# Kernel optimization log

Measured on AMD Instinct MI355X. Metric: run time of the kernel, lower is better.

The kernel has to match this reference:

```python
import jax, jax.numpy as jnp
import numpy as np

B, N, C = 64, 196, 768
H = 12
HD = C // H            # 64
TOPK = int(0.25 * HD)  # 16
HIDDEN = int(C * 4.0)  # 3072
SCALE = HD ** -0.5
EPS = 1e-5


def layernorm(x, g, b):
    mu = jnp.mean(x, axis=-1, keepdims=True)
    var = jnp.var(x, axis=-1, keepdims=True)
    return (x - mu) * jax.lax.rsqrt(var + EPS) * g + b


def setup_inputs() -> dict:
    key = jax.random.key(0)
    ks = jax.random.split(key, 8)
    s = 0.02
    return {
        "x": jax.random.normal(ks[0], (B, N, C), jnp.float32),
        "norm1_g": jnp.ones((C,), jnp.float32),
        "norm1_b": jnp.zeros((C,), jnp.float32),
        "qk_w": jax.random.normal(ks[1], (2 * C, C), jnp.float32) * s,   # torch Linear [out,in], no bias
        "attn_proj_w": jax.random.normal(ks[2], (C, H * TOPK), jnp.float32) * s,
        "attn_proj_b": jnp.zeros((C,), jnp.float32),
        "norm2_g": jnp.ones((C,), jnp.float32),
        "norm2_b": jnp.zeros((C,), jnp.float32),
        "fc1_w": jax.random.normal(ks[3], (HIDDEN, C), jnp.float32) * s,
        "fc1_b": jnp.zeros((HIDDEN,), jnp.float32),
        "fc2_w": jax.random.normal(ks[4], (C, HIDDEN), jnp.float32) * s,
        "fc2_b": jnp.zeros((C,), jnp.float32),
    }


def reference(x, norm1_g, norm1_b, qk_w, attn_proj_w, attn_proj_b,
              norm2_g, norm2_b, fc1_w, fc1_b, fc2_w, fc2_b):
    # --- HomoAttention branch ---
    h = layernorm(x, norm1_g, norm1_b)                       # [B,N,C]
    qk = h @ qk_w.T                                          # [B,N,2C]
    qk = qk.reshape(B, N, 2, H, HD).transpose(2, 0, 3, 1, 4) # [2,B,H,N,HD]
    q, k = qk[0] * SCALE, qk[1]
    attn = jnp.einsum('bhnd,bhmd->bhnm', q, k)               # [B,H,N,N]
    top_vals, _ = jax.lax.top_k(attn, TOPK)                  # [B,H,N,TOPK]
    a = jax.nn.softmax(top_vals, axis=-1)
    a = a.transpose(0, 2, 1, 3).reshape(B, N, H * TOPK)      # [B,N,H*TOPK]
    x = x + a @ attn_proj_w.T + attn_proj_b

    # --- MLP branch ---
    h2 = layernorm(x, norm2_g, norm2_b)
    h2 = jax.nn.gelu(h2 @ fc1_w.T + fc1_b, approximate=False)
    x = x + h2 @ fc2_w.T + fc2_b
    return x
```

## Files before the change

### kernel.cpp

```cpp
#include <hip/hip_runtime.h>


#define BATCH 64
#define SEQ   196
#define CH    768
#define NHEAD 12
#define HDIM  64
#define TOPK  16
#define HID   3072
#define MROWS 12544
#define MHALF 6272
#define SCALE_F 0.125f
#define NEGBIG -3e38f

typedef __bf16 bf16x8 __attribute__((ext_vector_type(8)));
typedef float  f32x4  __attribute__((ext_vector_type(4)));

__device__ __forceinline__ unsigned short f2b(float f) {
    union { float f; unsigned int i; } c; c.f = f;
    unsigned int u = c.i;
    return (unsigned short)((u + 0x7fffu + ((u >> 16) & 1u)) >> 16);
}

__device__ __forceinline__ void async16(const unsigned short* g, unsigned short* l) {
    __builtin_amdgcn_global_load_lds(
        (const __attribute__((address_space(1))) unsigned int*)(g),
        (__attribute__((address_space(3))) unsigned int*)(l), 16, 0, 0);
}

__global__ __launch_bounds__(256) void f2b4_k(const float* __restrict__ s0, unsigned short* __restrict__ d0, int n0,
                                              const float* __restrict__ s1, unsigned short* __restrict__ d1, int n1,
                                              const float* __restrict__ s2, unsigned short* __restrict__ d2, int n2,
                                              const float* __restrict__ s3, unsigned short* __restrict__ d3, int n3)
{
    int idx = (blockIdx.x * 256 + threadIdx.x) * 4;
    const float* s; unsigned short* d; int n;
    if (idx < n0) { s = s0; d = d0; n = n0; }
    else {
        idx -= n0;
        if (idx < n1) { s = s1; d = d1; n = n1; }
        else {
            idx -= n1;
            if (idx < n2) { s = s2; d = d2; n = n2; }
            else { idx -= n2; s = s3; d = d3; n = n3; }
        }
    }
    if (idx < n) {
        float4 v = *(const float4*)(s + idx);
        ushort4 o;
        o.x = f2b(v.x); o.y = f2b(v.y); o.z = f2b(v.z); o.w = f2b(v.w);
        *(ushort4*)(d + idx) = o;
    }
}

__global__ __launch_bounds__(256) void ln_k(const float* __restrict__ x,
                                            const float* __restrict__ gw,
                                            const float* __restrict__ bw,
                                            unsigned short* __restrict__ out)
{
    const int row = blockIdx.x;
    const int tid = threadIdx.x;
    const float* xr = x + (size_t)row * CH;
    float v0 = xr[tid], v1 = xr[tid + 256], v2 = xr[tid + 512];
    float s  = v0 + v1 + v2;
    float sq = v0*v0 + v1*v1 + v2*v2;
#pragma unroll
    for (int off = 32; off > 0; off >>= 1) {
        s  += __shfl_down(s, off, 64);
        sq += __shfl_down(sq, off, 64);
    }
    __shared__ __align__(16) float red[8];
    if ((tid & 63) == 0) { red[(tid >> 6) * 2] = s; red[(tid >> 6) * 2 + 1] = sq; }
    __syncthreads();
    s  = red[0] + red[2] + red[4] + red[6];
    sq = red[1] + red[3] + red[5] + red[7];
    float mu  = s * (1.0f / CH);
    float var = sq * (1.0f / CH) - mu * mu;
    float rs  = rsqrtf(var + 1e-5f);
    unsigned short* orow = out + (size_t)row * CH;
    orow[tid]       = f2b((v0 - mu) * rs * gw[tid]       + bw[tid]);
    orow[tid + 256] = f2b((v1 - mu) * rs * gw[tid + 256] + bw[tid + 256]);
    orow[tid + 512] = f2b((v2 - mu) * rs * gw[tid + 512] + bw[tid + 512]);
}

template<bool BIAS, bool RES, bool GELU, bool OUTF>
__global__ __launch_bounds__(256, 3)
void gemm_bt64(const unsigned short* __restrict__ A,
               const unsigned short* __restrict__ Bw,
               const float* __restrict__ bias,
               const float* __restrict__ resid,
               void* __restrict__ Cout,
               int M, int N, int K)
{
    __shared__ __align__(16) unsigned short As[2][2][64 * 32];
    __shared__ __align__(16) unsigned short Bs[2][2][128 * 32];
    const int tid  = threadIdx.x;
    const int w    = tid >> 6;
    const int lane = tid & 63;
    const int tileN = blockIdx.x * 128;
    const int tileM = blockIdx.y * 64;
    const int wn = w * 32;
    const int q   = lane >> 4;
    const int l16 = lane & 15;

    f32x4 acc[4][2];
#pragma unroll
    for (int i = 0; i < 4; ++i)
#pragma unroll
        for (int j = 0; j < 2; ++j) acc[i][j] = (f32x4){0.f, 0.f, 0.f, 0.f};

    const int r0 = tid >> 2, c0 = (tid & 3) * 8;

    const int kIters = K >> 6;

    auto stage = [&](int kt, int buf) {
#pragma unroll
        for (int h = 0; h < 2; ++h) {
            const size_t koff = (size_t)kt * 64 + h * 32;
            async16(A + (size_t)(tileM + r0) * K + koff + c0,
                    &As[buf][h][(size_t)(w * 64) * 8]);
            async16(Bw + (size_t)(tileN + r0) * K + koff + c0,
                    &Bs[buf][h][(size_t)(w * 64) * 8]);
            async16(Bw + (size_t)(tileN + r0 + 64) * K + koff + c0,
                    &Bs[buf][h][(size_t)(256 + w * 64) * 8]);
        }
    };

    stage(0, 0);
    int cur = 0;
    for (int kt = 0; kt < kIters; ++kt) {
        __syncthreads();
        if (kt + 1 < kIters) stage(kt + 1, cur ^ 1);
#pragma unroll
        for (int h = 0; h < 2; ++h) {
            bf16x8 af[4], bfr[2];
#pragma unroll
            for (int i = 0; i < 4; ++i)
                af[i] = *(const bf16x8*)&As[cur][h][(i * 16 + l16) * 32 + q * 8];
#pragma unroll
            for (int j = 0; j < 2; ++j)
                bfr[j] = *(const bf16x8*)&Bs[cur][h][(wn + j * 16 + l16) * 32 + q * 8];
#pragma unroll
            for (int i = 0; i < 4; ++i)
#pragma unroll
                for (int j = 0; j < 2; ++j)
                    acc[i][j] = __builtin_amdgcn_mfma_f32_16x16x32_bf16(af[i], bfr[j], acc[i][j], 0, 0, 0);
        }
        cur ^= 1;
    }

#pragma unroll
    for (int i = 0; i < 4; ++i) {
#pragma unroll
        for (int r = 0; r < 4; ++r) {
            int row = tileM + i * 16 + q * 4 + r;
#pragma unroll
            for (int j = 0; j < 2; ++j) {
                int col = tileN + wn + j * 16 + l16;
                float v = acc[i][j][r];
                if (BIAS) v += bias[col];
                if (GELU) v = 0.5f * v * (1.0f + erff(v * 0.70710678118f));
                if (RES)  v += resid[(size_t)row * N + col];
                if (OUTF) ((float*)Cout)[(size_t)row * N + col] = v;
                else      ((unsigned short*)Cout)[(size_t)row * N + col] = f2b(v);
            }
        }
    }
}

__global__ __launch_bounds__(256) void attn_topk(const unsigned short* __restrict__ qk,
                                                 unsigned short* __restrict__ aout)
{
    const int bh = blockIdx.x;
    const int b = bh / NHEAD, h = bh % NHEAD;
    __shared__ __align__(16) unsigned short Qs[208 * 64];
    __shared__ __align__(16) unsigned short Ks[208 * 64];
    const int tid = threadIdx.x;

    for (int i = tid; i < 208 * 8; i += 256) {
        int row = i >> 3, c = i & 7;
        uint4 vq = make_uint4(0, 0, 0, 0), vk = vq;
        if (row < SEQ) {
            const uint4* gp = (const uint4*)(qk + ((size_t)(b * SEQ + row) * 1536 + h * 64));
            vq = gp[c];
            vk = gp[c + 96];
        }
        int slot = c ^ (row & 7);
        *(uint4*)&Qs[row * 64 + slot * 8] = vq;
        *(uint4*)&Ks[row * 64 + slot * 8] = vk;
    }
    __syncthreads();

    const int w = tid >> 6, lane = tid & 63;
    const int q = lane >> 4, l16 = lane & 15;

    for (int tn = w; tn < 13; tn += 4) {
        const int nrow = tn * 16 + l16;
        const int nsw = nrow & 7;
        bf16x8 bq0 = *(const bf16x8*)&Qs[nrow * 64 + ((0 * 4 + q) ^ nsw) * 8];
        bf16x8 bq1 = *(const bf16x8*)&Qs[nrow * 64 + ((1 * 4 + q) ^ nsw) * 8];

        float t[TOPK];
#pragma unroll
        for (int j = 0; j < TOPK; ++j) t[j] = NEGBIG;

        for (int tm = 0; tm < 12; ++tm) {
            const int mrow = tm * 16 + l16;
            const int msw = mrow & 7;
            bf16x8 ak0 = *(const bf16x8*)&Ks[mrow * 64 + ((0 * 4 + q) ^ msw) * 8];
            bf16x8 ak1 = *(const bf16x8*)&Ks[mrow * 64 + ((1 * 4 + q) ^ msw) * 8];
            f32x4 acc = (f32x4){0.f, 0.f, 0.f, 0.f};
            acc = __builtin_amdgcn_mfma_f32_16x16x32_bf16(ak0, bq0, acc, 0, 0, 0);
            acc = __builtin_amdgcn_mfma_f32_16x16x32_bf16(ak1, bq1, acc, 0, 0, 0);
#pragma unroll
            for (int r = 0; r < 4; ++r) {
                float v = acc[r];
#pragma unroll
                for (int j = 0; j < TOPK; ++j) {
                    float mx = fmaxf(t[j], v);
                    v = fminf(t[j], v);
                    t[j] = mx;
                }
            }
        }
        {
            const int mrow = 12 * 16 + l16;
            const int msw = mrow & 7;
            bf16x8 ak0 = *(const bf16x8*)&Ks[mrow * 64 + ((0 * 4 + q) ^ msw) * 8];
            bf16x8 ak1 = *(const bf16x8*)&Ks[mrow * 64 + ((1 * 4 + q) ^ msw) * 8];
            f32x4 acc = (f32x4){0.f, 0.f, 0.f, 0.f};
            acc = __builtin_amdgcn_mfma_f32_16x16x32_bf16(ak0, bq0, acc, 0, 0, 0);
            acc = __builtin_amdgcn_mfma_f32_16x16x32_bf16(ak1, bq1, acc, 0, 0, 0);
#pragma unroll
            for (int r = 0; r < 4; ++r) {
                float v = (q == 0) ? acc[r] : NEGBIG;
#pragma unroll
                for (int j = 0; j < TOPK; ++j) {
                    float mx = fmaxf(t[j], v);
                    v = fminf(t[j], v);
                    t[j] = mx;
                }
            }
        }

#pragma unroll
        for (int stage = 0; stage < 2; ++stage) {
            const int xm = 16 << stage;
            float bl[TOPK], c[TOPK];
#pragma unroll
            for (int j = 0; j < TOPK; ++j) bl[j] = __shfl_xor(t[j], xm, 64);
#pragma unroll
            for (int j = 0; j < TOPK; ++j) c[j] = fmaxf(t[j], bl[TOPK - 1 - j]);
#pragma unroll
            for (int s = 8; s >= 1; s >>= 1) {
#pragma unroll
                for (int i = 0; i < TOPK; ++i) {
                    if ((i & s) == 0) {
                        float mx = fmaxf(c[i], c[i + s]);
                        c[i + s] = fminf(c[i], c[i + s]);
                        c[i] = mx;
                    }
                }
            }
#pragma unroll
            for (int j = 0; j < TOPK; ++j) t[j] = c[j];
        }

        if (q == 0 && nrow < SEQ) {
            float e[TOPK], sum = 0.f;
#pragma unroll
            for (int j = 0; j < TOPK; ++j) { e[j] = __expf((t[j] - t[0]) * SCALE_F); sum += e[j]; }
            float inv = 1.0f / sum;
            unsigned int pk[8];
#pragma unroll
            for (int jj = 0; jj < 8; ++jj)
                pk[jj] = (unsigned int)f2b(e[2 * jj] * inv) |
                         ((unsigned int)f2b(e[2 * jj + 1] * inv) << 16);
            unsigned short* dst = aout + ((size_t)(b * SEQ + nrow)) * (NHEAD * TOPK) + h * TOPK;
            ((uint4*)dst)[0] = make_uint4(pk[0], pk[1], pk[2], pk[3]);
            ((uint4*)dst)[1] = make_uint4(pk[4], pk[5], pk[6], pk[7]);
        }
    }
}

extern "C" void kernel_launch(void* const* d_in, const int* in_sizes, int n_in,
                              void* d_out, int out_size, void* d_ws, size_t ws_size,
                              hipStream_t stream)
{
    const float* x    = (const float*)d_in[0];
    const float* g1   = (const float*)d_in[1];
    const float* bb1  = (const float*)d_in[2];
    const float* qkw  = (const float*)d_in[3];
    const float* pw   = (const float*)d_in[4];
    const float* pb   = (const float*)d_in[5];
    const float* g2   = (const float*)d_in[6];
    const float* bb2  = (const float*)d_in[7];
    const float* f1w  = (const float*)d_in[8];
    const float* f1b  = (const float*)d_in[9];
    const float* f2w  = (const float*)d_in[10];
    const float* f2bp = (const float*)d_in[11];
    float* out = (float*)d_out;

    char* ws = (char*)d_ws;
    const size_t SZ_H   = (size_t)MROWS * CH * 2;
    const size_t N_WQK  = (size_t)2 * CH * CH;
    const size_t N_WP   = (size_t)CH * (NHEAD * TOPK);
    const size_t N_WF   = (size_t)HID * CH;
    const size_t SZ_W   = (N_WQK + N_WP + 2 * N_WF) * 2;
    const size_t SZ_A   = (size_t)MROWS * (NHEAD * TOPK) * 2;
    const size_t SZ_QK  = (size_t)MROWS * 2 * CH * 2;
    const size_t SZ_GGF = (size_t)MROWS * HID * 2;

    unsigned short* hbuf = (unsigned short*)(ws);
    unsigned short* wqk  = (unsigned short*)(ws + SZ_H);
    unsigned short* wp   = wqk + N_WQK;
    unsigned short* wf1  = wp  + N_WP;
    unsigned short* wf2  = wf1 + N_WF;
    unsigned short* av   = (unsigned short*)(ws + SZ_H + SZ_W);
    unsigned short* qk   = (unsigned short*)(ws + SZ_H + SZ_W + SZ_A);
    unsigned short* gg   = qk;
    float* x1 = out;

    const bool fullMLP = ws_size >= SZ_H + SZ_W + SZ_A + SZ_GGF;

    {
        int total4 = (int)((N_WQK + N_WP + 2 * N_WF) / 4);
        f2b4_k<<<(total4 + 255) / 256, 256, 0, stream>>>(
            qkw, wqk, (int)N_WQK, pw, wp, (int)N_WP,
            f1w, wf1, (int)N_WF, f2w, wf2, (int)N_WF);
    }

    ln_k<<<MROWS, 256, 0, stream>>>(x, g1, bb1, hbuf);
    gemm_bt64<false, false, false, false><<<dim3(2*CH/128, MROWS/64), 256, 0, stream>>>(
        hbuf, wqk, nullptr, nullptr, qk, MROWS, 2*CH, CH);
    attn_topk<<<BATCH * NHEAD, 256, 0, stream>>>(qk, av);
    gemm_bt64<true, true, false, true><<<dim3(CH/128, MROWS/64), 256, 0, stream>>>(
        av, wp, pb, x, x1, MROWS, CH, NHEAD*TOPK);
    ln_k<<<MROWS, 256, 0, stream>>>(x1, g2, bb2, hbuf);

    if (fullMLP) {
        gemm_bt64<true, false, true, false><<<dim3(HID/128, MROWS/64), 256, 0, stream>>>(
            hbuf, wf1, f1b, nullptr, gg, MROWS, HID, CH);
        gemm_bt64<true, true, false, true><<<dim3(CH/128, MROWS/64), 256, 0, stream>>>(
            gg, wf2, f2bp, x1, out, MROWS, CH, HID);
    } else {
        for (int half = 0; half < 2; ++half) {
            const size_t ro = (size_t)half * MHALF;
            gemm_bt64<true, false, true, false><<<dim3(HID/128, MHALF/64), 256, 0, stream>>>(
                hbuf + ro * CH, wf1, f1b, nullptr, gg, MHALF, HID, CH);
            gemm_bt64<true, true, false, true><<<dim3(CH/128, MHALF/64), 256, 0, stream>>>(
                gg, wf2, f2bp, x1 + ro * CH, out + ro * CH, MHALF, CH, HID);
        }
    }
}
```

Baseline: 476.5 us.

## Use 128-row GEMM tiles with XOR-swizzled LDS and 32-wide K steps

Templates the bf16 MFMA GEMM on the M tile size and uses 128x128 tiles, with a 2x2 warp layout of 64x64 warp tiles, for the QK and FC1 GEMMs. The projection and FC2 GEMMs keep 64-row tiles. Global-to-LDS loads now use an XOR swizzle on 16-byte chunks, and fragment reads undo it, to cut LDS bank conflicts. The K step per stage drops from 64 to 32 to keep LDS small, and launch bounds go up to 4 blocks per CU. The aim is more operand reuse per LDS byte and fewer bank conflicts, at the cost of twice as many barriers per K loop and more register pressure.

After: 468.5 us. Within noise of the previous version (-1.7%).

```diff
diff --git a/kernel.cpp b/kernel.cpp
--- a/kernel.cpp
+++ b/kernel.cpp
@@ -83,46 +83,49 @@
     orow[tid + 512] = f2b((v2 - mu) * rs * gw[tid + 512] + bw[tid + 512]);
 }
 
-template<bool BIAS, bool RES, bool GELU, bool OUTF>
-__global__ __launch_bounds__(256, 3)
-void gemm_bt64(const unsigned short* __restrict__ A,
-               const unsigned short* __restrict__ Bw,
-               const float* __restrict__ bias,
-               const float* __restrict__ resid,
-               void* __restrict__ Cout,
-               int M, int N, int K)
-{
-    __shared__ __align__(16) unsigned short As[2][2][64 * 32];
-    __shared__ __align__(16) unsigned short Bs[2][2][128 * 32];
+template<int TM, bool BIAS, bool RES, bool GELU, bool OUTF>
+__global__ __launch_bounds__(256, 4)
+void gemm_bt(const unsigned short* __restrict__ A,
+             const unsigned short* __restrict__ Bw,
+             const float* __restrict__ bias,
+             const float* __restrict__ resid,
+             void* __restrict__ Cout,
+             int M, int N, int K)
+{
+    constexpr int WCOLS = (TM == 128) ? 2 : 4;
+    constexpr int JF = 128 / (16 * WCOLS);
+    __shared__ __align__(16) unsigned short As[2][TM * 32];
+    __shared__ __align__(16) unsigned short Bs[2][128 * 32];
     const int tid  = threadIdx.x;
     const int w    = tid >> 6;
     const int lane = tid & 63;
     const int tileN = blockIdx.x * 128;
-    const int tileM = blockIdx.y * 64;
-    const int wn = w * 32;
+    const int tileM = blockIdx.y * TM;
+    const int wm = (w / WCOLS) * 64;
+    const int wn = (w % WCOLS) * (JF * 16);
     const int q   = lane >> 4;
     const int l16 = lane & 15;
-
-    f32x4 acc[4][2];
+    const int csw = (q ^ (l16 & 3)) * 8;
+
+    f32x4 acc[4][JF];
 #pragma unroll
     for (int i = 0; i < 4; ++i)
 #pragma unroll
-        for (int j = 0; j < 2; ++j) acc[i][j] = (f32x4){0.f, 0.f, 0.f, 0.f};
-
-    const int r0 = tid >> 2, c0 = (tid & 3) * 8;
-
-    const int kIters = K >> 6;
+        for (int j = 0; j < JF; ++j) acc[i][j] = (f32x4){0.f, 0.f, 0.f, 0.f};
+
+    const int r0 = tid >> 2;
+    const int g0 = ((tid & 3) ^ (r0 & 3)) * 8;
+    const int r1 = r0 + 64;
+
+    const int kIters = K >> 5;
 
     auto stage = [&](int kt, int buf) {
-#pragma unroll
-        for (int h = 0; h < 2; ++h) {
-            const size_t koff = (size_t)kt * 64 + h * 32;
-            async16(A + (size_t)(tileM + r0) * K + koff + c0,
-                    &As[buf][h][(size_t)(w * 64) * 8]);
-            async16(Bw + (size_t)(tileN + r0) * K + koff + c0,
-                    &Bs[buf][h][(size_t)(w * 64) * 8]);
-            async16(Bw + (size_t)(tileN + r0 + 64) * K + koff + c0,
-                    &Bs[buf][h][(size_t)(256 + w * 64) * 8]);
+        const size_t koff = (size_t)kt * 32 + g0;
+        async16(Bw + (size_t)(tileN + r0) * K + koff, &Bs[buf][(size_t)(w * 64) * 8]);
+        async16(Bw + (size_t)(tileN + r1) * K + koff, &Bs[buf][(size_t)(256 + w * 64) * 8]);
+        async16(A + (size_t)(tileM + r0) * K + koff, &As[buf][(size_t)(w * 64) * 8]);
+        if constexpr (TM == 128) {
+            async16(A + (size_t)(tileM + r1) * K + koff, &As[buf][(size_t)(256 + w * 64) * 8]);
         }
     };
 
@@ -131,21 +134,18 @@
     for (int kt = 0; kt < kIters; ++kt) {
         __syncthreads();
         if (kt + 1 < kIters) stage(kt + 1, cur ^ 1);
-#pragma unroll
-        for (int h = 0; h < 2; ++h) {
-            bf16x8 af[4], bfr[2];
-#pragma unroll
-            for (int i = 0; i < 4; ++i)
-                af[i] = *(const bf16x8*)&As[cur][h][(i * 16 + l16) * 32 + q * 8];
-#pragma unroll
-            for (int j = 0; j < 2; ++j)
-                bfr[j] = *(const bf16x8*)&Bs[cur][h][(wn + j * 16 + l16) * 32 + q * 8];
-#pragma unroll
-            for (int i = 0; i < 4; ++i)
-#pragma unroll
-                for (int j = 0; j < 2; ++j)
-                    acc[i][j] = __builtin_amdgcn_mfma_f32_16x16x32_bf16(af[i], bfr[j], acc[i][j], 0, 0, 0);
-        }
+        bf16x8 af[4], bfr[JF];
+#pragma unroll
+        for (int i = 0; i < 4; ++i)
+            af[i] = *(const bf16x8*)&As[cur][(wm + i * 16 + l16) * 32 + csw];
+#pragma unroll
+        for (int j = 0; j < JF; ++j)
+            bfr[j] = *(const bf16x8*)&Bs[cur][(wn + j * 16 + l16) * 32 + csw];
+#pragma unroll
+        for (int i = 0; i < 4; ++i)
+#pragma unroll
+            for (int j = 0; j < JF; ++j)
+                acc[i][j] = __builtin_amdgcn_mfma_f32_16x16x32_bf16(af[i], bfr[j], acc[i][j], 0, 0, 0);
         cur ^= 1;
     }
 
@@ -153,9 +153,9 @@
     for (int i = 0; i < 4; ++i) {
 #pragma unroll
         for (int r = 0; r < 4; ++r) {
-            int row = tileM + i * 16 + q * 4 + r;
-#pragma unroll
-            for (int j = 0; j < 2; ++j) {
+            int row = tileM + wm + i * 16 + q * 4 + r;
+#pragma unroll
+            for (int j = 0; j < JF; ++j) {
                 int col = tileN + wn + j * 16 + l16;
                 float v = acc[i][j][r];
                 if (BIAS) v += bias[col];
@@ -308,7 +308,6 @@
     const size_t N_WF   = (size_t)HID * CH;
     const size_t SZ_W   = (N_WQK + N_WP + 2 * N_WF) * 2;
     const size_t SZ_A   = (size_t)MROWS * (NHEAD * TOPK) * 2;
-    const size_t SZ_QK  = (size_t)MROWS * 2 * CH * 2;
     const size_t SZ_GGF = (size_t)MROWS * HID * 2;
 
     unsigned short* hbuf = (unsigned short*)(ws);
@@ -331,24 +330,24 @@
     }
 
     ln_k<<<MROWS, 256, 0, stream>>>(x, g1, bb1, hbuf);
-    gemm_bt64<false, false, false, false><<<dim3(2*CH/128, MROWS/64), 256, 0, stream>>>(
+    gemm_bt<128, false, false, false, false><<<dim3(2*CH/128, MROWS/128), 256, 0, stream>>>(
         hbuf, wqk, nullptr, nullptr, qk, MROWS, 2*CH, CH);
     attn_topk<<<BATCH * NHEAD, 256, 0, stream>>>(qk, av);
-    gemm_bt64<true, true, false, true><<<dim3(CH/128, MROWS/64), 256, 0, stream>>>(
+    gemm_bt<64, true, true, false, true><<<dim3(CH/128, MROWS/64), 256, 0, stream>>>(
         av, wp, pb, x, x1, MROWS, CH, NHEAD*TOPK);
     ln_k<<<MROWS, 256, 0, stream>>>(x1, g2, bb2, hbuf);
 
     if (fullMLP) {
-        gemm_bt64<true, false, true, false><<<dim3(HID/128, MROWS/64), 256, 0, stream>>>(
+        gemm_bt<128, true, false, true, false><<<dim3(HID/128, MROWS/128), 256, 0, stream>>>(
             hbuf, wf1, f1b, nullptr, gg, MROWS, HID, CH);
-        gemm_bt64<true, true, false, true><<<dim3(CH/128, MROWS/64), 256, 0, stream>>>(
+        gemm_bt<64, true, true, false, true><<<dim3(CH/128, MROWS/64), 256, 0, stream>>>(
             gg, wf2, f2bp, x1, out, MROWS, CH, HID);
     } else {
         for (int half = 0; half < 2; ++half) {
             const size_t ro = (size_t)half * MHALF;
-            gemm_bt64<true, false, true, false><<<dim3(HID/128, MHALF/64), 256, 0, stream>>>(
+            gemm_bt<128, true, false, true, false><<<dim3(HID/128, MHALF/128), 256, 0, stream>>>(
                 hbuf + ro * CH, wf1, f1b, nullptr, gg, MHALF, HID, CH);
-            gemm_bt64<true, true, false, true><<<dim3(CH/128, MHALF/64), 256, 0, stream>>>(
+            gemm_bt<64, true, true, false, true><<<dim3(CH/128, MHALF/64), 256, 0, stream>>>(
                 gg, wf2, f2bp, x1 + ro * CH, out + ro * CH, MHALF, CH, HID);
         }
     }
```
